# Optimization experiments

Measured on AMD Instinct MI355X. Metric: run time of the kernel, lower is better.

## Reference

```python
import jax, jax.numpy as jnp
import numpy as np

N_HEAD = 8
DQK = 64
DV = 64
D_IN = 512
D_OUT = 512
D_MID = 2048
B = 4
L = 2048
EPS = 1e-5


def layernorm(x):
    mu = jnp.mean(x, axis=-1, keepdims=True)
    var = jnp.mean(jnp.square(x - mu), axis=-1, keepdims=True)
    return (x - mu) / jnp.sqrt(var + EPS)


def setup_inputs() -> dict:
    key = jax.random.key(0)
    ks = jax.random.split(key, 10)
    s = 0.02
    return {
        "query": jax.random.normal(ks[0], (B, L, D_IN), jnp.float32),
        "key": jax.random.normal(ks[1], (B, L, D_IN), jnp.float32),
        "value": jax.random.normal(ks[2], (B, L, D_IN), jnp.float32),
        "mask": jnp.zeros((B, L, L), jnp.float32),
        "WQ": jax.random.normal(ks[3], (D_IN, N_HEAD * DQK), jnp.float32) * s,
        "WK": jax.random.normal(ks[4], (D_IN, N_HEAD * DQK), jnp.float32) * s,
        "WV": jax.random.normal(ks[5], (D_IN, N_HEAD * DV), jnp.float32) * s,
        "WO": jax.random.normal(ks[6], (N_HEAD * DV, D_OUT), jnp.float32) * s,
        "W1": jax.random.normal(ks[7], (D_OUT, D_MID), jnp.float32) * s,
        "W2": jax.random.normal(ks[8], (D_MID, D_OUT), jnp.float32) * s,
    }


def reference(query, key, value, mask, WQ, WK, WV, WO, W1, W2):
    bsz = query.shape[0]
    # projections -> [b, h, l, d]
    Q = (query @ WQ).reshape(bsz, -1, N_HEAD, DQK).transpose(0, 2, 1, 3)
    K = (key @ WK).reshape(bsz, -1, N_HEAD, DQK).transpose(0, 2, 1, 3)
    V = (value @ WV).reshape(bsz, -1, N_HEAD, DV).transpose(0, 2, 1, 3)
    # scaled dot-product attention with additive mask [b, 1, lq, lk]
    scores = jnp.einsum("bhqd,bhkd->bhqk", Q, K) / jnp.sqrt(jnp.float32(DQK))
    w = jax.nn.softmax(scores + mask[:, None, :, :], axis=-1)
    out = jnp.einsum("bhqk,bhkd->bhqd", w, V)
    out = out.transpose(0, 2, 1, 3).reshape(bsz, -1, N_HEAD * DV)
    out = out @ WO
    out = layernorm(query + out)
    ff = jax.nn.relu(out @ W1) @ W2
    return layernorm(out + ff)
```

## Files before the change

kernel.cpp:

```cpp
#include <hip/hip_runtime.h>
#include <hip/hip_bf16.h>

using bf16 = __bf16;
typedef __bf16 bf16x4 __attribute__((ext_vector_type(4)));
typedef __bf16 bf16x8 __attribute__((ext_vector_type(8)));
typedef float f32x4 __attribute__((ext_vector_type(4)));
typedef float f32x16 __attribute__((ext_vector_type(16)));
typedef unsigned uint2v __attribute__((ext_vector_type(2)));

static constexpr int BATCH = 4;
static constexpr int SEQ   = 2048;
static constexpr int DIN   = 512;
static constexpr int NHEAD = 8;
static constexpr int DMID  = 2048;
static constexpr int MROWS = BATCH * SEQ;

__device__ __forceinline__ void gload16(const void* g, void* l)
{
    __builtin_amdgcn_global_load_lds(
        (const __attribute__((address_space(1))) unsigned int*)g,
        (__attribute__((address_space(3))) unsigned int*)l, 16, 0, 0);
}

__device__ __forceinline__ unsigned cvtpk(float a, float b)
{
    unsigned r;
    asm("v_cvt_pk_bf16_f32 %0, %1, %2" : "=v"(r) : "v"(a), "v"(b));
    return r;
}

__global__ __launch_bounds__(256) void tw_mask(
    const float* __restrict__ WQ, const float* __restrict__ WK,
    const float* __restrict__ WV, const float* __restrict__ WO,
    const float* __restrict__ W1, const float* __restrict__ W2,
    bf16* __restrict__ WQt, bf16* __restrict__ WKt, bf16* __restrict__ WVt,
    bf16* __restrict__ WOt, bf16* __restrict__ W1t, bf16* __restrict__ W2t,
    const float* __restrict__ q, const float* __restrict__ k,
    const float* __restrict__ v,
    bf16* __restrict__ qb, bf16* __restrict__ kb, bf16* __restrict__ vb,
    const uint4* __restrict__ mask, int* __restrict__ flag)
{
    const int bid = blockIdx.x;
    if (bid >= 4096) {
        const int idx = bid - 4096;
        const float* src = idx < 1024 ? q : idx < 2048 ? k : v;
        bf16*       dst = idx < 1024 ? qb : idx < 2048 ? kb : vb;
        const size_t b4 = (size_t)(idx & 1023) * 1024;
#pragma unroll
        for (int i = 0; i < 4; ++i) {
            const float4 f = reinterpret_cast<const float4*>(src)[b4 + i * 256 + threadIdx.x];
            bf16x4 h;
            h[0] = (bf16)f.x; h[1] = (bf16)f.y; h[2] = (bf16)f.z; h[3] = (bf16)f.w;
            reinterpret_cast<bf16x4*>(dst)[b4 + i * 256 + threadIdx.x] = h;
        }
        return;
    }
    if (bid >= 3072) {
        const uint4* p = mask + (size_t)(bid - 3072) * 4096;
        unsigned nz = 0;
#pragma unroll
        for (int i = 0; i < 16; ++i) {
            const uint4 u = p[i * 256 + threadIdx.x];
            nz |= u.x | u.y | u.z | u.w;
        }
        if (nz) atomicOr(flag, 1);
        return;
    }
    __shared__ float tile[32][33];
    const float* in; bf16* out; int ip, op, cx, ry;
    if (bid < 1024) {
        const int w = bid >> 8, idx = bid & 255;
        in  = w == 0 ? WQ  : w == 1 ? WK  : w == 2 ? WV  : WO;
        out = w == 0 ? WQt : w == 1 ? WKt : w == 2 ? WVt : WOt;
        ip = 512; op = 512; cx = idx & 15; ry = idx >> 4;
    } else if (bid < 2048) {
        const int idx = bid - 1024;
        in = W1; out = W1t; ip = 2048; op = 512; cx = idx & 63; ry = idx >> 6;
    } else {
        const int idx = bid - 2048;
        in = W2; out = W2t; ip = 512; op = 2048; cx = idx & 15; ry = idx >> 4;
    }
    const int c0 = cx * 32, r0 = ry * 32;
    const int tx = threadIdx.x & 31, ty = threadIdx.x >> 5;
    for (int i = 0; i < 32; i += 8)
        tile[ty + i][tx] = in[(size_t)(r0 + ty + i) * ip + c0 + tx];
    __syncthreads();
    for (int i = 0; i < 32; i += 8)
        out[(size_t)(c0 + ty + i) * op + r0 + tx] = (bf16)tile[tx][ty + i];
}

template <int ACT>
__global__ __launch_bounds__(256) void gemm128(const bf16* __restrict__ A,
                                               const bf16* __restrict__ Bt,
                                               bf16* __restrict__ C,
                                               int N, int K)
{
    __shared__ bf16 sA[128 * 64];
    __shared__ bf16 sB[128 * 64];

    const int t    = threadIdx.x;
    const int lane = t & 63;
    const int wave = t >> 6;
    const int wm   = wave >> 1;
    const int wn   = wave & 1;
    const int lr   = lane & 15;
    const int lq   = lane >> 4;

    const int m0 = blockIdx.y * 128;
    const int n0 = blockIdx.x * 128;

    const int srow = lane >> 3;
    const int scol = (lane & 7) * 8;

    f32x4 acc[4][4] = {};

    for (int k0 = 0; k0 < K; k0 += 64) {
        if (k0) __syncthreads();
#pragma unroll
        for (int i = 0; i < 4; ++i) {
            const int ch = wave * 4 + i;
            const int r  = ch * 8 + srow;
            gload16(A  + (size_t)(m0 + r) * K + k0 + scol, sA + ch * 512);
            gload16(Bt + (size_t)(n0 + r) * K + k0 + scol, sB + ch * 512);
        }
        __syncthreads();

#pragma unroll
        for (int kk = 0; kk < 2; ++kk) {
            bf16x8 af[4], bfr[4];
#pragma unroll
            for (int x = 0; x < 4; ++x) {
                af[x]  = *reinterpret_cast<const bf16x8*>(&sA[(wm * 64 + x * 16 + lr) * 64 + kk * 32 + lq * 8]);
                bfr[x] = *reinterpret_cast<const bf16x8*>(&sB[(wn * 64 + x * 16 + lr) * 64 + kk * 32 + lq * 8]);
            }
#pragma unroll
            for (int m = 0; m < 4; ++m)
#pragma unroll
                for (int n = 0; n < 4; ++n)
                    acc[m][n] = __builtin_amdgcn_mfma_f32_16x16x32_bf16(af[m], bfr[n], acc[m][n], 0, 0, 0);
        }
    }

#pragma unroll
    for (int n = 0; n < 4; ++n) {
        const int col = n0 + wn * 64 + n * 16 + lr;
#pragma unroll
        for (int m = 0; m < 4; ++m) {
            const int rowb = m0 + wm * 64 + m * 16 + lq * 4;
#pragma unroll
            for (int j = 0; j < 4; ++j) {
                float v = acc[m][n][j];
                if (ACT == 1) v = v > 0.f ? v : 0.f;
                C[(size_t)(rowb + j) * N + col] = (bf16)v;
            }
        }
    }
}

__global__ __launch_bounds__(256) void gemm64_qkvb(const bf16* __restrict__ qb,
                                                   const bf16* __restrict__ kb,
                                                   const bf16* __restrict__ vb,
                                                   const bf16* __restrict__ WQt,
                                                   const bf16* __restrict__ WKt,
                                                   const bf16* __restrict__ WVt,
                                                   bf16* __restrict__ Qb,
                                                   bf16* __restrict__ Kb,
                                                   bf16* __restrict__ Vt)
{
    __shared__ bf16 sA[64 * 64];
    __shared__ bf16 sB[128 * 64];

    const bf16* A  = blockIdx.z == 0 ? qb  : blockIdx.z == 1 ? kb  : vb;
    const bf16* Bt = blockIdx.z == 0 ? WQt : blockIdx.z == 1 ? WKt : WVt;
    const int K = DIN;

    const int t    = threadIdx.x;
    const int lane = t & 63;
    const int wave = t >> 6;
    const int lr   = lane & 15;
    const int lq   = lane >> 4;

    const int m0 = blockIdx.y * 64;
    const int n0 = blockIdx.x * 128;

    const int srow = lane >> 3;
    const int scol = (lane & 7) * 8;

    f32x4 acc[4][2] = {};

    for (int k0 = 0; k0 < K; k0 += 64) {
        if (k0) __syncthreads();
#pragma unroll
        for (int i = 0; i < 2; ++i) {
            const int ch = wave * 2 + i;
            gload16(A + (size_t)(m0 + ch * 8 + srow) * K + k0 + scol, sA + ch * 512);
        }
#pragma unroll
        for (int i = 0; i < 4; ++i) {
            const int ch = wave * 4 + i;
            gload16(Bt + (size_t)(n0 + ch * 8 + srow) * K + k0 + scol, sB + ch * 512);
        }
        __syncthreads();

#pragma unroll
        for (int kk = 0; kk < 2; ++kk) {
            bf16x8 af[4], bfr[2];
#pragma unroll
            for (int x = 0; x < 4; ++x)
                af[x] = *reinterpret_cast<const bf16x8*>(&sA[(x * 16 + lr) * 64 + kk * 32 + lq * 8]);
#pragma unroll
            for (int n = 0; n < 2; ++n)
                bfr[n] = *reinterpret_cast<const bf16x8*>(&sB[(wave * 32 + n * 16 + lr) * 64 + kk * 32 + lq * 8]);
#pragma unroll
            for (int m = 0; m < 4; ++m)
#pragma unroll
                for (int n = 0; n < 2; ++n)
                    acc[m][n] = __builtin_amdgcn_mfma_f32_16x16x32_bf16(af[m], bfr[n], acc[m][n], 0, 0, 0);
        }
    }

    if (blockIdx.z < 2) {
        bf16* C = blockIdx.z == 0 ? Qb : Kb;
#pragma unroll
        for (int n = 0; n < 2; ++n) {
            const int col = n0 + wave * 32 + n * 16 + lr;
#pragma unroll
            for (int m = 0; m < 4; ++m) {
                const int rowb = m0 + m * 16 + lq * 4;
#pragma unroll
                for (int j = 0; j < 4; ++j)
                    C[(size_t)(rowb + j) * DIN + col] = (bf16)acc[m][n][j];
            }
        }
    } else {
        __syncthreads();
#pragma unroll
        for (int n = 0; n < 2; ++n)
#pragma unroll
            for (int m = 0; m < 4; ++m)
#pragma unroll
                for (int j = 0; j < 4; ++j)
                    sB[(wave * 32 + n * 16 + lr) * 64 + m * 16 + lq * 4 + j] = (bf16)acc[m][n][j];
        __syncthreads();
        const int c = t >> 1, half = t & 1;
#pragma unroll
        for (int qq = 0; qq < 4; ++qq) {
            const bf16x8 vv = *reinterpret_cast<const bf16x8*>(&sB[c * 64 + half * 32 + qq * 8]);
            *reinterpret_cast<bf16x8*>(Vt + (size_t)(n0 + c) * MROWS + m0 + half * 32 + qq * 8) = vv;
        }
    }
}

__global__ __launch_bounds__(256) void attn_kernel(const bf16* __restrict__ Qb,
                                                   const bf16* __restrict__ Kb,
                                                   const bf16* __restrict__ Vt,
                                                   const float* __restrict__ mask,
                                                   bf16* __restrict__ O,
                                                   const int* __restrict__ mzf)
{
    const int bi   = blockIdx.x;
    const int xcd  = bi & 7;
    const int slot = bi >> 3;
    const int pair = xcd * 4 + (slot >> 4);
    const int qt   = slot & 15;
    const int h    = pair >> 2;
    const int b    = pair & 3;

    const int t    = threadIdx.x;
    const int lane = t & 63;
    const int wave = t >> 6;
    const int l31  = lane & 31;
    const int hi   = lane >> 5;
    const int q0   = qt * 128;
    const bool useM = (*mzf != 0);

    __shared__ bf16 sK[64 * 64];
    __shared__ bf16 sV[64 * 64];
    __shared__ float sL[4][32];

    bf16x8 qf[4];
#pragma unroll
    for (int s = 0; s < 4; ++s)
        qf[s] = *reinterpret_cast<const bf16x8*>(
            Qb + (size_t)(b * SEQ + q0 + wave * 32 + l31) * DIN + h * 64 + s * 16 + hi * 8);

    f32x16 o0 = {}, o1 = {};
    float lacc = 0.f;

    const int sr = t >> 2;
    const int c1 = t & 3;

    const bf16* kbase = Kb + (size_t)(b * SEQ) * DIN + h * 64;
    const bf16* vbase = Vt + (size_t)(h * 64 + sr) * MROWS + b * SEQ;

    constexpr float L2E = 1.4426950408889634f;
    constexpr float SCL = 0.125f * L2E;

    int4 kr0 = *reinterpret_cast<const int4*>(kbase + (size_t)sr * DIN + c1 * 8);
    int4 kr1 = *reinterpret_cast<const int4*>(kbase + (size_t)sr * DIN + c1 * 8 + 32);
    int4 vr0 = *reinterpret_cast<const int4*>(vbase + c1 * 8);
    int4 vr1 = *reinterpret_cast<const int4*>(vbase + c1 * 8 + 32);

    for (int tile = 0; tile < SEQ / 64; ++tile) {
        if (tile) __syncthreads();

        {
            const int x = sr & 7;
            *reinterpret_cast<int4*>(&sK[sr * 64 + ((c1    ) ^ x) * 8]) = kr0;
            *reinterpret_cast<int4*>(&sK[sr * 64 + ((c1 + 4) ^ x) * 8]) = kr1;
            *reinterpret_cast<int4*>(&sV[sr * 64 + ((c1    ) ^ x) * 8]) = vr0;
            *reinterpret_cast<int4*>(&sV[sr * 64 + ((c1 + 4) ^ x) * 8]) = vr1;
        }

        if (tile + 1 < SEQ / 64) {
            const int k0 = (tile + 1) * 64;
            kr0 = *reinterpret_cast<const int4*>(kbase + (size_t)(k0 + sr) * DIN + c1 * 8);
            kr1 = *reinterpret_cast<const int4*>(kbase + (size_t)(k0 + sr) * DIN + c1 * 8 + 32);
            vr0 = *reinterpret_cast<const int4*>(vbase + k0 + c1 * 8);
            vr1 = *reinterpret_cast<const int4*>(vbase + k0 + c1 * 8 + 32);
        }
        __syncthreads();

        bf16x8 kf[2][4];
#pragma unroll
        for (int kb = 0; kb < 2; ++kb)
#pragma unroll
            for (int s = 0; s < 4; ++s) {
                const int r = kb * 32 + l31;
                kf[kb][s] = *reinterpret_cast<const bf16x8*>(
                    &sK[r * 64 + ((hi + 2 * s) ^ (r & 7)) * 8]);
            }
        bf16x8 vf[2][4];
#pragma unroll
        for (int dt = 0; dt < 2; ++dt)
#pragma unroll
            for (int c = 0; c < 4; ++c) {
                const int r = dt * 32 + l31;
                vf[dt][c] = *reinterpret_cast<const bf16x8*>(
                    &sV[r * 64 + ((hi + 2 * c) ^ (r & 7)) * 8]);
            }

        f32x16 st0 = {}, st1 = {};
#pragma unroll
        for (int s = 0; s < 4; ++s) {
            st0 = __builtin_amdgcn_mfma_f32_32x32x16_bf16(kf[0][s], qf[s], st0, 0, 0, 0);
            st1 = __builtin_amdgcn_mfma_f32_32x32x16_bf16(kf[1][s], qf[s], st1, 0, 0, 0);
        }

        float p[32];
        if (useM) {
            const float* mrow = mask + ((size_t)(b * SEQ + q0 + wave * 32 + l31)) * SEQ + tile * 64;
#pragma unroll
            for (int r = 0; r < 16; ++r) {
                const int kk = (r & 3) + 8 * (r >> 2) + 4 * hi;
                p[r]      = exp2f(st0[r] * SCL + mrow[kk]      * L2E);
                p[16 + r] = exp2f(st1[r] * SCL + mrow[32 + kk] * L2E);
            }
        } else {
#pragma unroll
            for (int r = 0; r < 16; ++r) {
                p[r]      = exp2f(st0[r] * SCL);
                p[16 + r] = exp2f(st1[r] * SCL);
            }
        }
#pragma unroll
        for (int r = 0; r < 32; ++r) lacc += p[r];

        bf16x8 pa[4];
#pragma unroll
        for (int c = 0; c < 4; ++c) {
            const int bse = c * 8;
            unsigned u0 = cvtpk(p[bse + 0], p[bse + 1]);
            unsigned u1 = cvtpk(p[bse + 2], p[bse + 3]);
            unsigned u2 = cvtpk(p[bse + 4], p[bse + 5]);
            unsigned u3 = cvtpk(p[bse + 6], p[bse + 7]);
            const uint2v r02 = __builtin_amdgcn_permlane32_swap(u0, u2, false, false);
            const uint2v r13 = __builtin_amdgcn_permlane32_swap(u1, u3, false, false);
            union { unsigned u[4]; bf16x8 v; } pk;
            pk.u[0] = r02.x; pk.u[1] = r13.x; pk.u[2] = r02.y; pk.u[3] = r13.y;
            pa[c] = pk.v;
        }

#pragma unroll
        for (int c = 0; c < 4; ++c) {
            o0 = __builtin_amdgcn_mfma_f32_32x32x16_bf16(pa[c], vf[0][c], o0, 0, 0, 0);
            o1 = __builtin_amdgcn_mfma_f32_32x32x16_bf16(pa[c], vf[1][c], o1, 0, 0, 0);
        }
    }

    lacc += __shfl_xor(lacc, 32);
    __syncthreads();
    if (lane < 32) sL[wave][lane] = lacc;
    __syncthreads();

#pragma unroll
    for (int r = 0; r < 16; ++r) {
        const int qr = (r & 3) + 8 * (r >> 2) + 4 * hi;
        const float inv = 1.f / sL[wave][qr];
        const size_t rowoff = (size_t)(b * SEQ + q0 + wave * 32 + qr) * DIN + h * 64;
        O[rowoff + l31]      = (bf16)(o0[r] * inv);
        O[rowoff + 32 + l31] = (bf16)(o1[r] * inv);
    }
}

__global__ __launch_bounds__(512) void gemm_ln(const bf16* __restrict__ A,
                                               const bf16* __restrict__ Bt,
                                               const float* __restrict__ X,
                                               bf16* __restrict__ Onb,
                                               float* __restrict__ Onf,
                                               int K)
{
    __shared__ bf16 sA[2][32 * 64];
    __shared__ bf16 sB[2][512 * 64];
    __shared__ float sRed[32][8];
    __shared__ float sMu[32];
    __shared__ float sRstd[32];

    const int t    = threadIdx.x;
    const int lane = t & 63;
    const int w    = t >> 6;
    const int lr   = lane & 15;
    const int lq   = lane >> 4;
    const int srow = lane >> 3;
    const int scol = (lane & 7) * 8;

    const int m0 = blockIdx.x * 32;

    auto stage = [&](int s, int b) {
        const int k0 = s * 64;
#pragma unroll
        for (int i = 0; i < 8; ++i) {
            const int ch = w * 8 + i;
            gload16(Bt + (size_t)(ch * 8 + srow) * K + k0 + scol, &sB[b][ch * 512]);
        }
        if (w < 4)
            gload16(A + (size_t)(m0 + w * 8 + srow) * K + k0 + scol, &sA[b][w * 512]);
    };

    f32x4 acc[2][4] = {};
    const int steps = K / 64;

    stage(0, 0);
    __syncthreads();

    for (int s = 0; s < steps; ++s) {
        const int b = s & 1;
        if (s + 1 < steps) stage(s + 1, b ^ 1);

#pragma unroll
        for (int kk = 0; kk < 2; ++kk) {
            bf16x8 af[2], bfr[4];
#pragma unroll
            for (int m = 0; m < 2; ++m)
                af[m] = *reinterpret_cast<const bf16x8*>(&sA[b][(m * 16 + lr) * 64 + kk * 32 + lq * 8]);
#pragma unroll
            for (int n = 0; n < 4; ++n)
                bfr[n] = *reinterpret_cast<const bf16x8*>(&sB[b][(w * 64 + n * 16 + lr) * 64 + kk * 32 + lq * 8]);
#pragma unroll
            for (int m = 0; m < 2; ++m)
#pragma unroll
                for (int n = 0; n < 4; ++n)
                    acc[m][n] = __builtin_amdgcn_mfma_f32_16x16x32_bf16(af[m], bfr[n], acc[m][n], 0, 0, 0);
        }
        __syncthreads();
    }

#pragma unroll
    for (int m = 0; m < 2; ++m)
#pragma unroll
        for (int n = 0; n < 4; ++n)
#pragma unroll
            for (int j = 0; j < 4; ++j)
                acc[m][n][j] += X[(size_t)(m0 + m * 16 + lq * 4 + j) * DIN + w * 64 + n * 16 + lr];

#pragma unroll
    for (int m = 0; m < 2; ++m)
#pragma unroll
        for (int j = 0; j < 4; ++j) {
            float s = acc[m][0][j] + acc[m][1][j] + acc[m][2][j] + acc[m][3][j];
            s += __shfl_xor(s, 1); s += __shfl_xor(s, 2);
            s += __shfl_xor(s, 4); s += __shfl_xor(s, 8);
            if (lr == 0) sRed[m * 16 + lq * 4 + j][w] = s;
        }
    __syncthreads();
    if (t < 32) {
        float s = 0.f;
#pragma unroll
        for (int ww = 0; ww < 8; ++ww) s += sRed[t][ww];
        sMu[t] = s * (1.f / DIN);
    }
    __syncthreads();

#pragma unroll
    for (int m = 0; m < 2; ++m)
#pragma unroll
        for (int j = 0; j < 4; ++j) {
            const float mu = sMu[m * 16 + lq * 4 + j];
            float s = 0.f;
#pragma unroll
            for (int n = 0; n < 4; ++n) {
                const float d = acc[m][n][j] - mu;
                s += d * d;
            }
            s += __shfl_xor(s, 1); s += __shfl_xor(s, 2);
            s += __shfl_xor(s, 4); s += __shfl_xor(s, 8);
            if (lr == 0) sRed[m * 16 + lq * 4 + j][w] = s;
        }
    __syncthreads();
    if (t < 32) {
        float s = 0.f;
#pragma unroll
        for (int ww = 0; ww < 8; ++ww) s += sRed[t][ww];
        sRstd[t] = rsqrtf(s * (1.f / DIN) + 1e-5f);
    }
    __syncthreads();

#pragma unroll
    for (int m = 0; m < 2; ++m)
#pragma unroll
        for (int j = 0; j < 4; ++j) {
            const int rl = m * 16 + lq * 4 + j;
            const float mu = sMu[rl], rstd = sRstd[rl];
            const size_t rowoff = (size_t)(m0 + rl) * DIN;
#pragma unroll
            for (int n = 0; n < 4; ++n) {
                const float r = (acc[m][n][j] - mu) * rstd;
                const int col = w * 64 + n * 16 + lr;
                if (Onb) Onb[rowoff + col] = (bf16)r;
                if (Onf) Onf[rowoff + col] = r;
            }
        }
}

extern "C" void kernel_launch(void* const* d_in, const int* in_sizes, int n_in,
                              void* d_out, int out_size, void* d_ws, size_t ws_size,
                              hipStream_t stream)
{
    const float* query = (const float*)d_in[0];
    const float* key   = (const float*)d_in[1];
    const float* value = (const float*)d_in[2];
    const float* mask  = (const float*)d_in[3];
    const float* WQ    = (const float*)d_in[4];
    const float* WK    = (const float*)d_in[5];
    const float* WV    = (const float*)d_in[6];
    const float* WO    = (const float*)d_in[7];
    const float* W1    = (const float*)d_in[8];
    const float* W2    = (const float*)d_in[9];

    char* w = (char*)d_ws;
    size_t off = 0;
    auto carve2 = [&](size_t elems) { bf16* p = (bf16*)(w + off); off += elems * 2; return p; };
    auto carve4 = [&](size_t elems) { float* p = (float*)(w + off); off += elems * 4; return p; };

    bf16* Qb    = carve2((size_t)MROWS * DIN);
    bf16* Kb    = carve2((size_t)MROWS * DIN);
    bf16* Vb    = carve2((size_t)MROWS * DIN);
    bf16* Vt    = carve2((size_t)MROWS * DIN);
    bf16* Mid   = carve2((size_t)MROWS * DMID);
    float* Ln1f = carve4((size_t)MROWS * DIN);
    bf16* WQt   = carve2((size_t)DIN * DIN);
    bf16* WKt   = carve2((size_t)DIN * DIN);
    bf16* WVt   = carve2((size_t)DIN * DIN);
    bf16* WOt   = carve2((size_t)DIN * DIN);
    bf16* W1t   = carve2((size_t)DIN * DMID);
    bf16* W2t   = carve2((size_t)DMID * DIN);
    int*  mzf   = (int*)(w + off); off += 16;
    if (off > ws_size) return;

    bf16* Ob   = Vb;
    bf16* Ln1b = Kb;
    bf16* qb = Mid;
    bf16* kb = Mid + (size_t)MROWS * DIN;
    bf16* vb = Mid + (size_t)2 * MROWS * DIN;

    const dim3 blk(256);

    hipMemsetAsync(mzf, 0, 4, stream);

    tw_mask<<<dim3(7168), blk, 0, stream>>>(WQ, WK, WV, WO, W1, W2,
                                            WQt, WKt, WVt, WOt, W1t, W2t,
                                            query, key, value, qb, kb, vb,
                                            (const uint4*)mask, mzf);

    gemm64_qkvb<<<dim3(DIN / 128, MROWS / 64, 3), blk, 0, stream>>>(qb, kb, vb,
                                                                    WQt, WKt, WVt, Qb, Kb, Vt);

    attn_kernel<<<dim3(512), blk, 0, stream>>>(Qb, Kb, Vt, mask, Ob, mzf);

    gemm_ln<<<dim3(MROWS / 32), dim3(512), 0, stream>>>(Ob, WOt, query, Ln1b, Ln1f, DIN);

    gemm128<1><<<dim3(DMID / 128, MROWS / 128), blk, 0, stream>>>(Ln1b, W1t, Mid, DMID, DIN);

    gemm_ln<<<dim3(MROWS / 32), dim3(512), 0, stream>>>(Mid, W2t, Ln1f,
                                                        (bf16*)nullptr, (float*)d_out, DMID);
}
```

Measured before the change: 359.6 us.

## Process 64 query rows per wave in attention to reuse K/V tiles

Each attention wave now handles two 32-row query groups, so a block covers 256 queries and the grid drops from 512 to 256 blocks. Each K/V tile staged in shared memory is reused for twice as many queries, which cuts K/V global and LDS traffic per query. The exp2f calls become a raw v_exp_f32 with an fma, the row sum uses a tree reduction, and the final barriers around the row-sum exchange are dropped. In exchange it doubles accumulator register pressure and leaves only one block per CU, so occupancy and latency hiding may suffer.

Result: faster. 350.3 us (-2.6%).

```diff
diff --git a/kernel.cpp b/kernel.cpp
--- a/kernel.cpp
+++ b/kernel.cpp
@@ -26,6 +26,13 @@
 {
     unsigned r;
     asm("v_cvt_pk_bf16_f32 %0, %1, %2" : "=v"(r) : "v"(a), "v"(b));
+    return r;
+}
+
+__device__ __forceinline__ float fexp2(float x)
+{
+    float r;
+    asm("v_exp_f32 %0, %1" : "=v"(r) : "v"(x));
     return r;
 }
 
@@ -261,8 +268,8 @@
     const int bi   = blockIdx.x;
     const int xcd  = bi & 7;
     const int slot = bi >> 3;
-    const int pair = xcd * 4 + (slot >> 4);
-    const int qt   = slot & 15;
+    const int pair = xcd * 4 + (slot >> 3);
+    const int qt   = slot & 7;
     const int h    = pair >> 2;
     const int b    = pair & 3;
 
@@ -271,21 +278,23 @@
     const int wave = t >> 6;
     const int l31  = lane & 31;
     const int hi   = lane >> 5;
-    const int q0   = qt * 128;
+    const int q0   = qt * 256;
     const bool useM = (*mzf != 0);
 
     __shared__ bf16 sK[64 * 64];
     __shared__ bf16 sV[64 * 64];
-    __shared__ float sL[4][32];
-
-    bf16x8 qf[4];
-#pragma unroll
-    for (int s = 0; s < 4; ++s)
-        qf[s] = *reinterpret_cast<const bf16x8*>(
-            Qb + (size_t)(b * SEQ + q0 + wave * 32 + l31) * DIN + h * 64 + s * 16 + hi * 8);
-
-    f32x16 o0 = {}, o1 = {};
-    float lacc = 0.f;
+    __shared__ float sL[4][64];
+
+    bf16x8 qf[2][4];
+#pragma unroll
+    for (int g = 0; g < 2; ++g)
+#pragma unroll
+        for (int s = 0; s < 4; ++s)
+            qf[g][s] = *reinterpret_cast<const bf16x8*>(
+                Qb + (size_t)(b * SEQ + q0 + wave * 64 + g * 32 + l31) * DIN + h * 64 + s * 16 + hi * 8);
+
+    f32x16 o[2][2] = {};
+    float lacc[2] = {};
 
     const int sr = t >> 2;
     const int c1 = t & 3;
@@ -340,67 +349,84 @@
                     &sV[r * 64 + ((hi + 2 * c) ^ (r & 7)) * 8]);
             }
 
-        f32x16 st0 = {}, st1 = {};
-#pragma unroll
-        for (int s = 0; s < 4; ++s) {
-            st0 = __builtin_amdgcn_mfma_f32_32x32x16_bf16(kf[0][s], qf[s], st0, 0, 0, 0);
-            st1 = __builtin_amdgcn_mfma_f32_32x32x16_bf16(kf[1][s], qf[s], st1, 0, 0, 0);
-        }
-
-        float p[32];
-        if (useM) {
-            const float* mrow = mask + ((size_t)(b * SEQ + q0 + wave * 32 + l31)) * SEQ + tile * 64;
-#pragma unroll
-            for (int r = 0; r < 16; ++r) {
-                const int kk = (r & 3) + 8 * (r >> 2) + 4 * hi;
-                p[r]      = exp2f(st0[r] * SCL + mrow[kk]      * L2E);
-                p[16 + r] = exp2f(st1[r] * SCL + mrow[32 + kk] * L2E);
-            }
-        } else {
-#pragma unroll
-            for (int r = 0; r < 16; ++r) {
-                p[r]      = exp2f(st0[r] * SCL);
-                p[16 + r] = exp2f(st1[r] * SCL);
-            }
-        }
-#pragma unroll
-        for (int r = 0; r < 32; ++r) lacc += p[r];
-
-        bf16x8 pa[4];
-#pragma unroll
-        for (int c = 0; c < 4; ++c) {
-            const int bse = c * 8;
-            unsigned u0 = cvtpk(p[bse + 0], p[bse + 1]);
-            unsigned u1 = cvtpk(p[bse + 2], p[bse + 3]);
-            unsigned u2 = cvtpk(p[bse + 4], p[bse + 5]);
-            unsigned u3 = cvtpk(p[bse + 6], p[bse + 7]);
-            const uint2v r02 = __builtin_amdgcn_permlane32_swap(u0, u2, false, false);
-            const uint2v r13 = __builtin_amdgcn_permlane32_swap(u1, u3, false, false);
-            union { unsigned u[4]; bf16x8 v; } pk;
-            pk.u[0] = r02.x; pk.u[1] = r13.x; pk.u[2] = r02.y; pk.u[3] = r13.y;
-            pa[c] = pk.v;
-        }
-
-#pragma unroll
-        for (int c = 0; c < 4; ++c) {
-            o0 = __builtin_amdgcn_mfma_f32_32x32x16_bf16(pa[c], vf[0][c], o0, 0, 0, 0);
-            o1 = __builtin_amdgcn_mfma_f32_32x32x16_bf16(pa[c], vf[1][c], o1, 0, 0, 0);
-        }
-    }
-
-    lacc += __shfl_xor(lacc, 32);
-    __syncthreads();
-    if (lane < 32) sL[wave][lane] = lacc;
-    __syncthreads();
-
-#pragma unroll
-    for (int r = 0; r < 16; ++r) {
-        const int qr = (r & 3) + 8 * (r >> 2) + 4 * hi;
-        const float inv = 1.f / sL[wave][qr];
-        const size_t rowoff = (size_t)(b * SEQ + q0 + wave * 32 + qr) * DIN + h * 64;
-        O[rowoff + l31]      = (bf16)(o0[r] * inv);
-        O[rowoff + 32 + l31] = (bf16)(o1[r] * inv);
-    }
+#pragma unroll
+        for (int g = 0; g < 2; ++g) {
+            f32x16 st0 = {}, st1 = {};
+#pragma unroll
+            for (int s = 0; s < 4; ++s) {
+                st0 = __builtin_amdgcn_mfma_f32_32x32x16_bf16(kf[0][s], qf[g][s], st0, 0, 0, 0);
+                st1 = __builtin_amdgcn_mfma_f32_32x32x16_bf16(kf[1][s], qf[g][s], st1, 0, 0, 0);
+            }
+
+            float p[32];
+            if (useM) {
+                const float* mrow = mask + ((size_t)(b * SEQ + q0 + wave * 64 + g * 32 + l31)) * SEQ + tile * 64;
+#pragma unroll
+                for (int r = 0; r < 16; ++r) {
+                    const int kk = (r & 3) + 8 * (r >> 2) + 4 * hi;
+                    p[r]      = fexp2(fmaf(st0[r], SCL, mrow[kk]      * L2E));
+                    p[16 + r] = fexp2(fmaf(st1[r], SCL, mrow[32 + kk] * L2E));
+                }
+            } else {
+#pragma unroll
+                for (int r = 0; r < 16; ++r) {
+                    p[r]      = fexp2(st0[r] * SCL);
+                    p[16 + r] = fexp2(st1[r] * SCL);
+                }
+            }
+            {
+                float s0 = 0.f, s1 = 0.f, s2 = 0.f, s3 = 0.f;
+#pragma unroll
+                for (int r = 0; r < 8; ++r) {
+                    s0 += p[r];
+                    s1 += p[8 + r];
+                    s2 += p[16 + r];
+                    s3 += p[24 + r];
+                }
+                lacc[g] += (s0 + s1) + (s2 + s3);
+            }
+
+            bf16x8 pa[4];
+#pragma unroll
+            for (int c = 0; c < 4; ++c) {
+                const int bse = c * 8;
+                unsigned u0 = cvtpk(p[bse + 0], p[bse + 1]);
+                unsigned u1 = cvtpk(p[bse + 2], p[bse + 3]);
+                unsigned u2 = cvtpk(p[bse + 4], p[bse + 5]);
+                unsigned u3 = cvtpk(p[bse + 6], p[bse + 7]);
+                const uint2v r02 = __builtin_amdgcn_permlane32_swap(u0, u2, false, false);
+                const uint2v r13 = __builtin_amdgcn_permlane32_swap(u1, u3, false, false);
+                union { unsigned u[4]; bf16x8 v; } pk;
+                pk.u[0] = r02.x; pk.u[1] = r13.x; pk.u[2] = r02.y; pk.u[3] = r13.y;
+                pa[c] = pk.v;
+            }
+
+#pragma unroll
+            for (int c = 0; c < 4; ++c) {
+                o[g][0] = __builtin_amdgcn_mfma_f32_32x32x16_bf16(pa[c], vf[0][c], o[g][0], 0, 0, 0);
+                o[g][1] = __builtin_amdgcn_mfma_f32_32x32x16_bf16(pa[c], vf[1][c], o[g][1], 0, 0, 0);
+            }
+        }
+    }
+
+#pragma unroll
+    for (int g = 0; g < 2; ++g)
+        lacc[g] += __shfl_xor(lacc[g], 32);
+    if (hi == 0) {
+        sL[wave][l31]      = lacc[0];
+        sL[wave][32 + l31] = lacc[1];
+    }
+
+#pragma unroll
+    for (int g = 0; g < 2; ++g)
+#pragma unroll
+        for (int r = 0; r < 16; ++r) {
+            const int qr = (r & 3) + 8 * (r >> 2) + 4 * hi;
+            const float inv = 1.f / sL[wave][g * 32 + qr];
+            const size_t rowoff = (size_t)(b * SEQ + q0 + wave * 64 + g * 32 + qr) * DIN + h * 64;
+            O[rowoff + l31]      = (bf16)(o[g][0][r] * inv);
+            O[rowoff + 32 + l31] = (bf16)(o[g][1][r] * inv);
+        }
 }
 
 __global__ __launch_bounds__(512) void gemm_ln(const bf16* __restrict__ A,
@@ -585,7 +611,7 @@
     gemm64_qkvb<<<dim3(DIN / 128, MROWS / 64, 3), blk, 0, stream>>>(qb, kb, vb,
                                                                     WQt, WKt, WVt, Qb, Kb, Vt);
 
-    attn_kernel<<<dim3(512), blk, 0, stream>>>(Qb, Kb, Vt, mask, Ob, mzf);
+    attn_kernel<<<dim3(256), blk, 0, stream>>>(Qb, Kb, Vt, mask, Ob, mzf);
 
     gemm_ln<<<dim3(MROWS / 32), dim3(512), 0, stream>>>(Ob, WOt, query, Ln1b, Ln1f, DIN);
 
```
